# Performance work log

Measured on AMD Instinct MI355X. Metric: run time of the kernel, lower is better.

## Reference

```python
import jax, jax.numpy as jnp
import numpy as np

N, E = 50000, 1600000
IN, OUT, H = 128, 32, 2
NT, ET = 20, 4
ETE, EAE, ED = 16, 16, 16
SLOPE = 0.2  # conv_neg_slope


def setup_inputs() -> dict:
    key = jax.random.key(0)
    ks = jax.random.split(key, 11)
    d_att = 2 * OUT + ETE + EAE
    return dict(
        x=jax.random.normal(ks[0], (N, IN), jnp.float32),
        edge_index=jax.random.randint(ks[1], (2, E), 0, N),
        ntypes=jax.random.randint(ks[2], (N,), 0, NT),
        etypes=jax.random.randint(ks[3], (E,), 0, ET),
        eattr=jax.random.normal(ks[4], (E, ED), jnp.float32),
        het_W=jax.random.normal(ks[5], (NT, IN, OUT), jnp.float32) / np.sqrt(IN).astype(np.float32),
        het_b=jnp.zeros((NT, OUT), jnp.float32),
        etype_table=jax.random.normal(ks[6], (ET, ETE), jnp.float32),
        eattr_W=jax.random.normal(ks[7], (ED, EAE), jnp.float32) / np.sqrt(ED).astype(np.float32),
        att_W=jax.random.normal(ks[8], (d_att, H), jnp.float32) / np.sqrt(d_att).astype(np.float32),
        lin_W=jax.random.normal(ks[9], (OUT + EAE, OUT), jnp.float32) / np.sqrt(OUT + EAE).astype(np.float32),
    )


def _lrelu(v):
    return jax.nn.leaky_relu(v, SLOPE)


def _heat_conv(x, edge_index, ntypes, etypes, eattr,
               het_W, het_b, etype_table, eattr_W, att_W, lin_W):
    # HeteroLinear: node-type-conditioned linear transform (loop over 20 types,
    # avoids materializing a [N, IN, OUT] gathered-weight tensor)
    h = jnp.zeros((x.shape[0], het_W.shape[-1]), x.dtype)
    for t in range(het_W.shape[0]):
        h = h + jnp.where((ntypes == t)[:, None], x @ het_W[t] + het_b[t], 0.0)

    src, dst = edge_index[0], edge_index[1]
    ete = _lrelu(etype_table[etypes])        # [E, ETE] edge-type embedding
    ea = _lrelu(eattr @ eattr_W)             # [E, EAE] edge-attr embedding
    x_i = h[dst]                             # target node feats [E, OUT]
    x_j = h[src]                             # source node feats [E, OUT]

    feat = jnp.concatenate([x_i, x_j, ete, ea], axis=-1)
    alpha = _lrelu(feat @ att_W)             # [E, H] raw attention logits

    # softmax grouped by destination node, per head
    amax = jax.ops.segment_max(alpha, dst, num_segments=N)  # [N, H]
    alpha = jnp.exp(alpha - amax[dst])
    denom = jax.ops.segment_sum(alpha, dst, num_segments=N)  # [N, H]
    alpha = alpha / denom[dst]

    msg = jnp.concatenate([x_j, ea], axis=-1) @ lin_W        # [E, OUT]
    m = (msg[:, None, :] * alpha[:, :, None]).reshape(alpha.shape[0], H * OUT)
    out = jax.ops.segment_sum(m, dst, num_segments=N)        # [N, H*OUT]
    return out  # concat=True -> flattened heads


def reference(x, edge_index, ntypes, etypes, eattr,
              het_W, het_b, etype_table, eattr_W, att_W, lin_W):
    out = _heat_conv(x, edge_index, ntypes, etypes, eattr,
                     het_W, het_b, etype_table, eattr_W, att_W, lin_W)
    return jax.nn.relu(out)  # final activation in forward (eval mode: no dropout)
```

## Files before the change

kernel.cpp:

```cpp
#include <hip/hip_runtime.h>
#include <hip/hip_fp16.h>

#define NN 50000
#define EE 1600000
#define IN_F 128
#define OUT_F 32
#define SLOPE 0.2f
#define NB_SCAN 196

__global__ __launch_bounds__(256) void k_node(
    const float* __restrict__ x, const int* __restrict__ ntypes,
    const float* __restrict__ hetW, const float* __restrict__ hetb,
    const float* __restrict__ linW, const float* __restrict__ attW,
    float* __restrict__ hlin, float* __restrict__ auxS,
    float* __restrict__ auxD)
{
    __shared__ float sH[32 * 33];
    __shared__ float sLin[32 * 32];
    int tid = threadIdx.x;
    for (int i = tid; i < 1024; i += 256) sLin[i] = linW[i];

    int g = tid >> 3;
    int j = tid & 7;
    int n = blockIdx.x * 32 + g;
    int nc = n < NN ? n : NN - 1;
    int t = ntypes[nc];
    const float* W = hetW + (size_t)t * (IN_F * OUT_F);
    const float4* xr = (const float4*)(x + (size_t)nc * IN_F);

    float4 acc = ((const float4*)(hetb + t * OUT_F))[j];
    #pragma unroll 4
    for (int c = 0; c < 32; ++c) {
        float4 xv = xr[c];
        const float* Wr = W + (4 * c) * OUT_F + 4 * j;
        float4 w0 = *(const float4*)(Wr);
        float4 w1 = *(const float4*)(Wr + OUT_F);
        float4 w2 = *(const float4*)(Wr + 2 * OUT_F);
        float4 w3 = *(const float4*)(Wr + 3 * OUT_F);
        acc.x += xv.x * w0.x + xv.y * w1.x + xv.z * w2.x + xv.w * w3.x;
        acc.y += xv.x * w0.y + xv.y * w1.y + xv.z * w2.y + xv.w * w3.y;
        acc.z += xv.x * w0.z + xv.y * w1.z + xv.z * w2.z + xv.w * w3.z;
        acc.w += xv.x * w0.w + xv.y * w1.w + xv.z * w2.w + xv.w * w3.w;
    }
    sH[g * 33 + 4 * j + 0] = acc.x;
    sH[g * 33 + 4 * j + 1] = acc.y;
    sH[g * 33 + 4 * j + 2] = acc.z;
    sH[g * 33 + 4 * j + 3] = acc.w;
    __syncthreads();

    int o = tid & 31;
    #pragma unroll
    for (int pass = 0; pass < 4; ++pass) {
        int g2 = (tid >> 5) + 8 * pass;
        int n2 = blockIdx.x * 32 + g2;
        if (n2 >= NN) break;
        float accl = 0.0f;
        #pragma unroll
        for (int k = 0; k < 32; ++k)
            accl += sH[g2 * 33 + k] * sLin[k * 32 + o];
        hlin[(size_t)n2 * 32 + o] = accl;

        float hv = sH[g2 * 33 + o];
        float p0 = hv * attW[o * 2],        p1 = hv * attW[o * 2 + 1];
        float p2 = hv * attW[(32 + o) * 2], p3 = hv * attW[(32 + o) * 2 + 1];
        #pragma unroll
        for (int m = 16; m >= 1; m >>= 1) {
            p0 += __shfl_xor(p0, m, 32);
            p1 += __shfl_xor(p1, m, 32);
            p2 += __shfl_xor(p2, m, 32);
            p3 += __shfl_xor(p3, m, 32);
        }
        if (o == 0) {
            auxD[n2 * 2] = p0; auxD[n2 * 2 + 1] = p1;
            auxS[n2 * 2] = p2; auxS[n2 * 2 + 1] = p3;
        }
    }
}

__global__ __launch_bounds__(256) void k_count(
    const int* __restrict__ dst, int* __restrict__ count)
{
    int e = blockIdx.x * 256 + threadIdx.x;
    atomicAdd(&count[dst[e]], 1);
}

__global__ __launch_bounds__(256) void k_scanA(
    const int* __restrict__ count, int* __restrict__ offsets,
    int* __restrict__ bsum)
{
    __shared__ int s[256];
    int t = threadIdx.x;
    int i = blockIdx.x * 256 + t;
    int c = (i < NN) ? count[i] : 0;
    s[t] = c;
    __syncthreads();
    for (int off = 1; off < 256; off <<= 1) {
        int v = (t >= off) ? s[t - off] : 0;
        __syncthreads();
        s[t] += v;
        __syncthreads();
    }
    if (i < NN) offsets[i] = s[t] - c;
    if (t == 255) bsum[blockIdx.x] = s[255];
}

__global__ __launch_bounds__(256) void k_scanB(
    const int* __restrict__ bsum, int* __restrict__ bbase,
    const float* __restrict__ etab, const float* __restrict__ attW,
    float* __restrict__ etedot)
{
    __shared__ int s[256];
    int t = threadIdx.x;
    if (t < 8) {
        int et = t >> 1, hh = t & 1;
        float acc = 0.0f;
        for (int k = 0; k < 16; ++k) {
            float v = etab[et * 16 + k];
            v = v > 0.0f ? v : SLOPE * v;
            acc += v * attW[(64 + k) * 2 + hh];
        }
        etedot[t] = acc;
    }
    int c = (t < NB_SCAN) ? bsum[t] : 0;
    s[t] = c;
    __syncthreads();
    for (int off = 1; off < 256; off <<= 1) {
        int v = (t >= off) ? s[t - off] : 0;
        __syncthreads();
        s[t] += v;
        __syncthreads();
    }
    if (t < NB_SCAN) bbase[t] = s[t] - c;
}

__global__ __launch_bounds__(256) void k_scanC(
    int* __restrict__ offsets, const int* __restrict__ bbase,
    int* __restrict__ next)
{
    int t = threadIdx.x;
    int i = blockIdx.x * 256 + t;
    if (i < NN) {
        int v = offsets[i] + bbase[blockIdx.x];
        offsets[i] = v;
        next[i] = v;
    }
    if (i == 0) offsets[NN] = EE;
}

__global__ __launch_bounds__(256) void k_pre(
    const int* __restrict__ srcp, const int* __restrict__ dstp,
    const int* __restrict__ etypes, const float* __restrict__ eattr,
    const float* __restrict__ eaW, const float* __restrict__ attW,
    const float* __restrict__ etedot, const float* __restrict__ auxS,
    const float* __restrict__ auxD, int* __restrict__ next,
    int* __restrict__ srcS, int* __restrict__ dstS,
    float2* __restrict__ pS, __half* __restrict__ eaS)
{
    int e = blockIdx.x * 256 + threadIdx.x;
    int s = srcp[e], d = dstp[e], et = etypes[e];
    int slot = atomicAdd(&next[d], 1);

    float attr[16];
    {
        const float4* ap = (const float4*)(eattr + (size_t)e * 16);
        #pragma unroll
        for (int q = 0; q < 4; ++q) {
            float4 v = ap[q];
            attr[4*q+0] = v.x; attr[4*q+1] = v.y;
            attr[4*q+2] = v.z; attr[4*q+3] = v.w;
        }
    }
    float ea[16];
    #pragma unroll
    for (int j = 0; j < 16; ++j) {
        float acc = 0.0f;
        #pragma unroll
        for (int k = 0; k < 16; ++k) acc += attr[k] * eaW[k * 16 + j];
        ea[j] = acc > 0.0f ? acc : SLOPE * acc;
    }

    float2 aD = ((const float2*)auxD)[d];
    float2 aS = ((const float2*)auxS)[s];
    float2 eD = ((const float2*)etedot)[et];
    float al0 = aD.x + aS.x + eD.x;
    float al1 = aD.y + aS.y + eD.y;
    #pragma unroll
    for (int j = 0; j < 16; ++j) {
        al0 += ea[j] * attW[(80 + j) * 2];
        al1 += ea[j] * attW[(80 + j) * 2 + 1];
    }
    al0 = al0 > 0.0f ? al0 : SLOPE * al0;
    al1 = al1 > 0.0f ? al1 : SLOPE * al1;
    float p0 = __expf(al0), p1 = __expf(al1);

    srcS[slot] = s;
    dstS[slot] = d;
    pS[slot] = make_float2(p0, p1);
    __half2 eh[8];
    #pragma unroll
    for (int q = 0; q < 8; ++q) eh[q] = __floats2half2_rn(ea[2*q], ea[2*q+1]);
    float4* ep = (float4*)(eaS + (size_t)slot * 16);
    const float4* es = (const float4*)eh;
    ep[0] = es[0];
    ep[1] = es[1];
}

__global__ __launch_bounds__(256) void k_main2(
    const int* __restrict__ offsets, const int* __restrict__ srcS,
    const int* __restrict__ dstS, const float2* __restrict__ pS,
    const __half* __restrict__ eaS, const float* __restrict__ linW,
    const float* __restrict__ hlin,
    float* __restrict__ out, float* __restrict__ numbuf,
    float* __restrict__ denombuf)
{
    __shared__ float sMsg[256 * 33];
    __shared__ float sP[256 * 2];
    __shared__ int   sDst[256];
    __shared__ int   sWCnt[4];
    __shared__ int   sSegStart[256];
    __shared__ int   sSegNode[256];

    int tid = threadIdx.x;
    int s = blockIdx.x * 256 + tid;
    int src = srcS[s];
    int d   = dstS[s];
    float2 pp = pS[s];
    sDst[tid] = d;
    sP[tid * 2 + 0] = pp.x;
    sP[tid * 2 + 1] = pp.y;

    float ea[16];
    {
        const float4* ep = (const float4*)(eaS + (size_t)s * 16);
        float4 r0 = ep[0], r1 = ep[1];
        const __half2* eh0 = (const __half2*)&r0;
        const __half2* eh1 = (const __half2*)&r1;
        #pragma unroll
        for (int q = 0; q < 4; ++q) {
            float2 v = __half22float2(eh0[q]);
            ea[2*q] = v.x; ea[2*q+1] = v.y;
        }
        #pragma unroll
        for (int q = 0; q < 4; ++q) {
            float2 v = __half22float2(eh1[q]);
            ea[8+2*q] = v.x; ea[8+2*q+1] = v.y;
        }
    }

    float msg[32];
    {
        const float4* hp = (const float4*)(hlin + (size_t)src * 32);
        #pragma unroll
        for (int q = 0; q < 8; ++q) {
            float4 v = hp[q];
            msg[4*q+0] = v.x; msg[4*q+1] = v.y;
            msg[4*q+2] = v.z; msg[4*q+3] = v.w;
        }
    }
    #pragma unroll
    for (int j = 0; j < 16; ++j) {
        float e = ea[j];
        #pragma unroll
        for (int o = 0; o < 32; ++o) msg[o] += e * linW[(32 + j) * 32 + o];
    }
    #pragma unroll
    for (int o = 0; o < 32; ++o) sMsg[tid * 33 + o] = msg[o];
    __syncthreads();

    int ln = tid & 63, wv = tid >> 6;
    bool isStart = (tid == 0) || (sDst[tid - 1] != d);
    unsigned long long bm = __ballot(isStart);
    int wrank = __popcll(bm & ((1ull << ln) - 1ull));
    if (ln == 0) sWCnt[wv] = __popcll(bm);
    __syncthreads();
    int base = 0, nSeg = 0;
    #pragma unroll
    for (int w = 0; w < 4; ++w) {
        int c = sWCnt[w];
        if (w < wv) base += c;
        nSeg += c;
    }
    if (isStart) {
        int sid = base + wrank;
        sSegStart[sid] = tid;
        sSegNode[sid] = d;
    }
    __syncthreads();

    int o = ln & 31, hh = ln >> 5;
    int gs = blockIdx.x * 256;
    for (int g = wv; g < nSeg; g += 4) {
        int a = sSegStart[g];
        int b = (g + 1 < nSeg) ? sSegStart[g + 1] : 256;
        int n = sSegNode[g];
        float accm = 0.0f, accp = 0.0f;
        for (int tt = a; tt < b; ++tt) {
            float p = sP[tt * 2 + hh];
            accm += p * sMsg[tt * 33 + o];
            accp += p;
        }
        int o0 = offsets[n], o1 = offsets[n + 1];
        bool interior = (o0 == gs + a) && (o1 == gs + b);
        if (interior) {
            float v = accm / accp;
            out[(size_t)n * 64 + ln] = v > 0.0f ? v : 0.0f;
            if (o == 0) denombuf[n * 2 + hh] = -1.0f;
        } else {
            atomicAdd(&numbuf[(size_t)n * 64 + ln], accm);
            if (o == 0) atomicAdd(&denombuf[n * 2 + hh], accp);
        }
    }
}

__global__ __launch_bounds__(256) void k_final(
    float* __restrict__ out, const float* __restrict__ numbuf,
    const float* __restrict__ denombuf)
{
    int i = blockIdx.x * 256 + threadIdx.x;
    int n = i >> 6;
    int hh = (i >> 5) & 1;
    float dn = denombuf[n * 2 + hh];
    if (dn > 0.0f) {
        float v = numbuf[i] / dn;
        out[i] = v > 0.0f ? v : 0.0f;
    } else if (dn == 0.0f) {
        out[i] = 0.0f;
    }
}

extern "C" void kernel_launch(void* const* d_in, const int* in_sizes, int n_in,
                              void* d_out, int out_size, void* d_ws, size_t ws_size,
                              hipStream_t stream)
{
    const float* x      = (const float*)d_in[0];
    const int*   eidx   = (const int*)  d_in[1];
    const int*   ntypes = (const int*)  d_in[2];
    const int*   etypes = (const int*)  d_in[3];
    const float* eattr  = (const float*)d_in[4];
    const float* hetW   = (const float*)d_in[5];
    const float* hetb   = (const float*)d_in[6];
    const float* etab   = (const float*)d_in[7];
    const float* eaW    = (const float*)d_in[8];
    const float* attW   = (const float*)d_in[9];
    const float* linW   = (const float*)d_in[10];
    float* out = (float*)d_out;

    char* ws = (char*)d_ws;
    size_t off = 0;
    auto alloc = [&](size_t bytes) {
        char* p = ws + off;
        off = (off + bytes + 255) & ~(size_t)255;
        return p;
    };
    float*  hlin     = (float*) alloc((size_t)NN * 32 * sizeof(float));
    float*  auxS     = (float*) alloc((size_t)NN * 2 * sizeof(float));
    float*  auxD     = (float*) alloc((size_t)NN * 2 * sizeof(float));
    float*  etedot   = (float*) alloc(8 * sizeof(float));
    int*    count    = (int*)   alloc((size_t)NN * sizeof(int));
    int*    offsets  = (int*)   alloc(((size_t)NN + 1) * sizeof(int));
    int*    next     = (int*)   alloc((size_t)NN * sizeof(int));
    int*    bsum     = (int*)   alloc(256 * sizeof(int));
    int*    bbase    = (int*)   alloc(256 * sizeof(int));
    int*    srcS     = (int*)   alloc((size_t)EE * sizeof(int));
    int*    dstS     = (int*)   alloc((size_t)EE * sizeof(int));
    float2* pS       = (float2*)alloc((size_t)EE * sizeof(float2));
    __half* eaS      = (__half*)alloc((size_t)EE * 16 * sizeof(__half));
    float*  numbuf   = (float*) alloc((size_t)NN * 64 * sizeof(float));
    float*  denombuf = (float*) alloc((size_t)NN * 2 * sizeof(float));
    (void)ws_size;

    const int* srcp = eidx;
    const int* dstp = eidx + EE;

    hipMemsetAsync(count,    0, (size_t)NN * sizeof(int), stream);
    hipMemsetAsync(numbuf,   0, (size_t)NN * 64 * sizeof(float), stream);
    hipMemsetAsync(denombuf, 0, (size_t)NN * 2 * sizeof(float), stream);

    k_node<<<(NN + 31) / 32, 256, 0, stream>>>(x, ntypes, hetW, hetb, linW,
                                               attW, hlin, auxS, auxD);
    k_count<<<EE / 256, 256, 0, stream>>>(dstp, count);
    k_scanA<<<NB_SCAN, 256, 0, stream>>>(count, offsets, bsum);
    k_scanB<<<1, 256, 0, stream>>>(bsum, bbase, etab, attW, etedot);
    k_scanC<<<NB_SCAN, 256, 0, stream>>>(offsets, bbase, next);
    k_pre<<<EE / 256, 256, 0, stream>>>(srcp, dstp, etypes, eattr, eaW, attW,
                                        etedot, auxS, auxD, next,
                                        srcS, dstS, pS, eaS);
    k_main2<<<EE / 256, 256, 0, stream>>>(offsets, srcS, dstS, pS, eaS, linW,
                                          hlin, out, numbuf, denombuf);
    k_final<<<(NN * 64) / 256, 256, 0, stream>>>(out, numbuf, denombuf);
}
```

Baseline: 536.8 us.

## Replace per-node CSR sort with coarse bucket partition and shared-memory accumulation

Replaces the per-destination count/scan/scatter and the segmented reduction with a coarse bucketing scheme of 128 destination nodes per bucket. A single partition pass computes the full fp16 message and the attention weights, then writes a packed 80-byte payload per edge, using block-local ranks plus one global atomic per bucket. A second kernel accumulates each bucket in shared memory with LDS atomics and normalizes and ReLUs directly into the output. This removes the global numbuf/denombuf atomics, the final kernel and several launches, at the cost of a larger payload write and heavy LDS atomic contention in the accumulation pass.

Measured after the change: 1.125 ms. 110% more time.

```diff
diff --git a/kernel.cpp b/kernel.cpp
--- a/kernel.cpp
+++ b/kernel.cpp
@@ -4,9 +4,12 @@
 #define NN 50000
 #define EE 1600000
 #define IN_F 128
-#define OUT_F 32
 #define SLOPE 0.2f
-#define NB_SCAN 196
+#define BSH 7
+#define BNODES 128
+#define NBUCK 391
+#define P1_CHUNK 4096
+#define NB_P1 391
 
 __global__ __launch_bounds__(256) void k_node(
     const float* __restrict__ x, const int* __restrict__ ntypes,
@@ -25,18 +28,18 @@
     int n = blockIdx.x * 32 + g;
     int nc = n < NN ? n : NN - 1;
     int t = ntypes[nc];
-    const float* W = hetW + (size_t)t * (IN_F * OUT_F);
+    const float* W = hetW + (size_t)t * (IN_F * 32);
     const float4* xr = (const float4*)(x + (size_t)nc * IN_F);
 
-    float4 acc = ((const float4*)(hetb + t * OUT_F))[j];
+    float4 acc = ((const float4*)(hetb + t * 32))[j];
     #pragma unroll 4
     for (int c = 0; c < 32; ++c) {
         float4 xv = xr[c];
-        const float* Wr = W + (4 * c) * OUT_F + 4 * j;
+        const float* Wr = W + (4 * c) * 32 + 4 * j;
         float4 w0 = *(const float4*)(Wr);
-        float4 w1 = *(const float4*)(Wr + OUT_F);
-        float4 w2 = *(const float4*)(Wr + 2 * OUT_F);
-        float4 w3 = *(const float4*)(Wr + 3 * OUT_F);
+        float4 w1 = *(const float4*)(Wr + 32);
+        float4 w2 = *(const float4*)(Wr + 64);
+        float4 w3 = *(const float4*)(Wr + 96);
         acc.x += xv.x * w0.x + xv.y * w1.x + xv.z * w2.x + xv.w * w3.x;
         acc.y += xv.x * w0.y + xv.y * w1.y + xv.z * w2.y + xv.w * w3.y;
         acc.z += xv.x * w0.z + xv.y * w1.z + xv.z * w2.z + xv.w * w3.z;
@@ -77,39 +80,30 @@
     }
 }
 
-__global__ __launch_bounds__(256) void k_count(
-    const int* __restrict__ dst, int* __restrict__ count)
-{
-    int e = blockIdx.x * 256 + threadIdx.x;
-    atomicAdd(&count[dst[e]], 1);
-}
-
-__global__ __launch_bounds__(256) void k_scanA(
-    const int* __restrict__ count, int* __restrict__ offsets,
-    int* __restrict__ bsum)
-{
-    __shared__ int s[256];
-    int t = threadIdx.x;
-    int i = blockIdx.x * 256 + t;
-    int c = (i < NN) ? count[i] : 0;
-    s[t] = c;
-    __syncthreads();
-    for (int off = 1; off < 256; off <<= 1) {
-        int v = (t >= off) ? s[t - off] : 0;
-        __syncthreads();
-        s[t] += v;
-        __syncthreads();
-    }
-    if (i < NN) offsets[i] = s[t] - c;
-    if (t == 255) bsum[blockIdx.x] = s[255];
-}
-
-__global__ __launch_bounds__(256) void k_scanB(
-    const int* __restrict__ bsum, int* __restrict__ bbase,
-    const float* __restrict__ etab, const float* __restrict__ attW,
-    float* __restrict__ etedot)
-{
-    __shared__ int s[256];
+__global__ __launch_bounds__(512) void k_bhist(
+    const int* __restrict__ dst, int* __restrict__ bcount)
+{
+    __shared__ int lh[NBUCK];
+    int tid = threadIdx.x;
+    for (int i = tid; i < NBUCK; i += 512) lh[i] = 0;
+    __syncthreads();
+    int e0 = blockIdx.x * P1_CHUNK;
+    #pragma unroll
+    for (int k = 0; k < 8; ++k) {
+        int e = e0 + k * 512 + tid;
+        if (e < EE) atomicAdd(&lh[dst[e] >> BSH], 1);
+    }
+    __syncthreads();
+    for (int i = tid; i < NBUCK; i += 512)
+        if (lh[i]) atomicAdd(&bcount[i], lh[i]);
+}
+
+__global__ __launch_bounds__(512) void k_bscan(
+    const int* __restrict__ bcount, int* __restrict__ bbase,
+    int* __restrict__ cursor, const float* __restrict__ etab,
+    const float* __restrict__ attW, float* __restrict__ etedot)
+{
+    __shared__ int s[512];
     int t = threadIdx.x;
     if (t < 8) {
         int et = t >> 1, hh = t & 1;
@@ -121,210 +115,170 @@
         }
         etedot[t] = acc;
     }
-    int c = (t < NB_SCAN) ? bsum[t] : 0;
+    int c = (t < NBUCK) ? bcount[t] : 0;
     s[t] = c;
     __syncthreads();
-    for (int off = 1; off < 256; off <<= 1) {
+    for (int off = 1; off < 512; off <<= 1) {
         int v = (t >= off) ? s[t - off] : 0;
         __syncthreads();
         s[t] += v;
         __syncthreads();
     }
-    if (t < NB_SCAN) bbase[t] = s[t] - c;
-}
-
-__global__ __launch_bounds__(256) void k_scanC(
-    int* __restrict__ offsets, const int* __restrict__ bbase,
-    int* __restrict__ next)
-{
-    int t = threadIdx.x;
-    int i = blockIdx.x * 256 + t;
-    if (i < NN) {
-        int v = offsets[i] + bbase[blockIdx.x];
-        offsets[i] = v;
-        next[i] = v;
-    }
-    if (i == 0) offsets[NN] = EE;
-}
-
-__global__ __launch_bounds__(256) void k_pre(
+    if (t < NBUCK) {
+        int b = s[t] - c;
+        bbase[t] = b;
+        cursor[t] = b;
+    }
+    if (t == 0) bbase[NBUCK] = EE;
+}
+
+__global__ __launch_bounds__(512) void k_p1(
     const int* __restrict__ srcp, const int* __restrict__ dstp,
     const int* __restrict__ etypes, const float* __restrict__ eattr,
     const float* __restrict__ eaW, const float* __restrict__ attW,
-    const float* __restrict__ etedot, const float* __restrict__ auxS,
-    const float* __restrict__ auxD, int* __restrict__ next,
-    int* __restrict__ srcS, int* __restrict__ dstS,
-    float2* __restrict__ pS, __half* __restrict__ eaS)
-{
-    int e = blockIdx.x * 256 + threadIdx.x;
-    int s = srcp[e], d = dstp[e], et = etypes[e];
-    int slot = atomicAdd(&next[d], 1);
-
-    float attr[16];
-    {
-        const float4* ap = (const float4*)(eattr + (size_t)e * 16);
-        #pragma unroll
-        for (int q = 0; q < 4; ++q) {
-            float4 v = ap[q];
-            attr[4*q+0] = v.x; attr[4*q+1] = v.y;
-            attr[4*q+2] = v.z; attr[4*q+3] = v.w;
-        }
-    }
-    float ea[16];
+    const float* __restrict__ linW, const float* __restrict__ etedot,
+    const float* __restrict__ auxS, const float* __restrict__ auxD,
+    const float* __restrict__ hlin, int* __restrict__ cursor,
+    float4* __restrict__ payload)
+{
+    __shared__ int lh[NBUCK];
+    __shared__ int lbase[NBUCK];
+    int tid = threadIdx.x;
+    for (int i = tid; i < NBUCK; i += 512) lh[i] = 0;
+    __syncthreads();
+
+    int e0 = blockIdx.x * P1_CHUNK;
+    int myrank[8], myb[8];
     #pragma unroll
-    for (int j = 0; j < 16; ++j) {
-        float acc = 0.0f;
-        #pragma unroll
-        for (int k = 0; k < 16; ++k) acc += attr[k] * eaW[k * 16 + j];
-        ea[j] = acc > 0.0f ? acc : SLOPE * acc;
-    }
-
-    float2 aD = ((const float2*)auxD)[d];
-    float2 aS = ((const float2*)auxS)[s];
-    float2 eD = ((const float2*)etedot)[et];
-    float al0 = aD.x + aS.x + eD.x;
-    float al1 = aD.y + aS.y + eD.y;
-    #pragma unroll
-    for (int j = 0; j < 16; ++j) {
-        al0 += ea[j] * attW[(80 + j) * 2];
-        al1 += ea[j] * attW[(80 + j) * 2 + 1];
-    }
-    al0 = al0 > 0.0f ? al0 : SLOPE * al0;
-    al1 = al1 > 0.0f ? al1 : SLOPE * al1;
-    float p0 = __expf(al0), p1 = __expf(al1);
-
-    srcS[slot] = s;
-    dstS[slot] = d;
-    pS[slot] = make_float2(p0, p1);
-    __half2 eh[8];
-    #pragma unroll
-    for (int q = 0; q < 8; ++q) eh[q] = __floats2half2_rn(ea[2*q], ea[2*q+1]);
-    float4* ep = (float4*)(eaS + (size_t)slot * 16);
-    const float4* es = (const float4*)eh;
-    ep[0] = es[0];
-    ep[1] = es[1];
-}
-
-__global__ __launch_bounds__(256) void k_main2(
-    const int* __restrict__ offsets, const int* __restrict__ srcS,
-    const int* __restrict__ dstS, const float2* __restrict__ pS,
-    const __half* __restrict__ eaS, const float* __restrict__ linW,
-    const float* __restrict__ hlin,
-    float* __restrict__ out, float* __restrict__ numbuf,
-    float* __restrict__ denombuf)
-{
-    __shared__ float sMsg[256 * 33];
-    __shared__ float sP[256 * 2];
-    __shared__ int   sDst[256];
-    __shared__ int   sWCnt[4];
-    __shared__ int   sSegStart[256];
-    __shared__ int   sSegNode[256];
-
+    for (int k = 0; k < 8; ++k) {
+        int e = e0 + k * 512 + tid;
+        if (e >= EE) break;
+        int b = dstp[e] >> BSH;
+        myb[k] = b;
+        myrank[k] = atomicAdd(&lh[b], 1);
+    }
+    __syncthreads();
+    for (int i = tid; i < NBUCK; i += 512) {
+        int c = lh[i];
+        lbase[i] = c ? atomicAdd(&cursor[i], c) : 0;
+    }
+    __syncthreads();
+
+    for (int k = 0; k < 8; ++k) {
+        int e = e0 + k * 512 + tid;
+        if (e >= EE) break;
+        int s = srcp[e], d = dstp[e], et = etypes[e];
+
+        float attr[16];
+        {
+            const float4* ap = (const float4*)(eattr + (size_t)e * 16);
+            #pragma unroll
+            for (int q = 0; q < 4; ++q) {
+                float4 v = ap[q];
+                attr[4*q+0] = v.x; attr[4*q+1] = v.y;
+                attr[4*q+2] = v.z; attr[4*q+3] = v.w;
+            }
+        }
+        float ea[16];
+        #pragma unroll
+        for (int j = 0; j < 16; ++j) {
+            float acc = 0.0f;
+            #pragma unroll
+            for (int kk = 0; kk < 16; ++kk) acc += attr[kk] * eaW[kk * 16 + j];
+            ea[j] = acc > 0.0f ? acc : SLOPE * acc;
+        }
+
+        float2 aD = ((const float2*)auxD)[d];
+        float2 aS = ((const float2*)auxS)[s];
+        float2 eD = ((const float2*)etedot)[et];
+        float al0 = aD.x + aS.x + eD.x;
+        float al1 = aD.y + aS.y + eD.y;
+        #pragma unroll
+        for (int j = 0; j < 16; ++j) {
+            al0 += ea[j] * attW[(80 + j) * 2];
+            al1 += ea[j] * attW[(80 + j) * 2 + 1];
+        }
+        al0 = al0 > 0.0f ? al0 : SLOPE * al0;
+        al1 = al1 > 0.0f ? al1 : SLOPE * al1;
+        float p0 = __expf(al0), p1 = __expf(al1);
+
+        float msg[32];
+        {
+            const float4* hp = (const float4*)(hlin + (size_t)s * 32);
+            #pragma unroll
+            for (int q = 0; q < 8; ++q) {
+                float4 v = hp[q];
+                msg[4*q+0] = v.x; msg[4*q+1] = v.y;
+                msg[4*q+2] = v.z; msg[4*q+3] = v.w;
+            }
+        }
+        #pragma unroll
+        for (int j = 0; j < 16; ++j) {
+            float ej = ea[j];
+            #pragma unroll
+            for (int o = 0; o < 32; ++o) msg[o] += ej * linW[(32 + j) * 32 + o];
+        }
+
+        int slot = lbase[myb[k]] + myrank[k];
+        float4* P = payload + (size_t)slot * 5;
+        P[0] = make_float4(__int_as_float(d & (BNODES - 1)), p0, p1, 0.0f);
+        __half2 mh[16];
+        #pragma unroll
+        for (int q = 0; q < 16; ++q)
+            mh[q] = __floats2half2_rn(msg[2*q], msg[2*q+1]);
+        const float4* ms = (const float4*)mh;
+        P[1] = ms[0]; P[2] = ms[1]; P[3] = ms[2]; P[4] = ms[3];
+    }
+}
+
+__global__ __launch_bounds__(512) void k_p2(
+    const float4* __restrict__ payload, const int* __restrict__ bbase,
+    float* __restrict__ out)
+{
+    __shared__ float sNum[BNODES * 65];
+    __shared__ float sDen[BNODES * 2];
     int tid = threadIdx.x;
-    int s = blockIdx.x * 256 + tid;
-    int src = srcS[s];
-    int d   = dstS[s];
-    float2 pp = pS[s];
-    sDst[tid] = d;
-    sP[tid * 2 + 0] = pp.x;
-    sP[tid * 2 + 1] = pp.y;
-
-    float ea[16];
-    {
-        const float4* ep = (const float4*)(eaS + (size_t)s * 16);
-        float4 r0 = ep[0], r1 = ep[1];
-        const __half2* eh0 = (const __half2*)&r0;
-        const __half2* eh1 = (const __half2*)&r1;
-        #pragma unroll
-        for (int q = 0; q < 4; ++q) {
-            float2 v = __half22float2(eh0[q]);
-            ea[2*q] = v.x; ea[2*q+1] = v.y;
-        }
-        #pragma unroll
-        for (int q = 0; q < 4; ++q) {
-            float2 v = __half22float2(eh1[q]);
-            ea[8+2*q] = v.x; ea[8+2*q+1] = v.y;
-        }
-    }
-
-    float msg[32];
-    {
-        const float4* hp = (const float4*)(hlin + (size_t)src * 32);
-        #pragma unroll
-        for (int q = 0; q < 8; ++q) {
-            float4 v = hp[q];
-            msg[4*q+0] = v.x; msg[4*q+1] = v.y;
-            msg[4*q+2] = v.z; msg[4*q+3] = v.w;
-        }
-    }
-    #pragma unroll
-    for (int j = 0; j < 16; ++j) {
-        float e = ea[j];
-        #pragma unroll
-        for (int o = 0; o < 32; ++o) msg[o] += e * linW[(32 + j) * 32 + o];
-    }
-    #pragma unroll
-    for (int o = 0; o < 32; ++o) sMsg[tid * 33 + o] = msg[o];
-    __syncthreads();
-
-    int ln = tid & 63, wv = tid >> 6;
-    bool isStart = (tid == 0) || (sDst[tid - 1] != d);
-    unsigned long long bm = __ballot(isStart);
-    int wrank = __popcll(bm & ((1ull << ln) - 1ull));
-    if (ln == 0) sWCnt[wv] = __popcll(bm);
-    __syncthreads();
-    int base = 0, nSeg = 0;
-    #pragma unroll
-    for (int w = 0; w < 4; ++w) {
-        int c = sWCnt[w];
-        if (w < wv) base += c;
-        nSeg += c;
-    }
-    if (isStart) {
-        int sid = base + wrank;
-        sSegStart[sid] = tid;
-        sSegNode[sid] = d;
-    }
-    __syncthreads();
-
-    int o = ln & 31, hh = ln >> 5;
-    int gs = blockIdx.x * 256;
-    for (int g = wv; g < nSeg; g += 4) {
-        int a = sSegStart[g];
-        int b = (g + 1 < nSeg) ? sSegStart[g + 1] : 256;
-        int n = sSegNode[g];
-        float accm = 0.0f, accp = 0.0f;
-        for (int tt = a; tt < b; ++tt) {
-            float p = sP[tt * 2 + hh];
-            accm += p * sMsg[tt * 33 + o];
-            accp += p;
-        }
-        int o0 = offsets[n], o1 = offsets[n + 1];
-        bool interior = (o0 == gs + a) && (o1 == gs + b);
-        if (interior) {
-            float v = accm / accp;
-            out[(size_t)n * 64 + ln] = v > 0.0f ? v : 0.0f;
-            if (o == 0) denombuf[n * 2 + hh] = -1.0f;
-        } else {
-            atomicAdd(&numbuf[(size_t)n * 64 + ln], accm);
-            if (o == 0) atomicAdd(&denombuf[n * 2 + hh], accp);
-        }
-    }
-}
-
-__global__ __launch_bounds__(256) void k_final(
-    float* __restrict__ out, const float* __restrict__ numbuf,
-    const float* __restrict__ denombuf)
-{
-    int i = blockIdx.x * 256 + threadIdx.x;
-    int n = i >> 6;
-    int hh = (i >> 5) & 1;
-    float dn = denombuf[n * 2 + hh];
-    if (dn > 0.0f) {
-        float v = numbuf[i] / dn;
-        out[i] = v > 0.0f ? v : 0.0f;
-    } else if (dn == 0.0f) {
-        out[i] = 0.0f;
+    for (int i = tid; i < BNODES * 65; i += 512) sNum[i] = 0.0f;
+    for (int i = tid; i < BNODES * 2; i += 512) sDen[i] = 0.0f;
+    __syncthreads();
+
+    int b = blockIdx.x;
+    int s0 = bbase[b], s1 = bbase[b + 1];
+
+    for (int e = s0 + tid; e < s1; e += 512) {
+        const float4* P = payload + (size_t)e * 5;
+        float4 h0 = P[0];
+        float4 r0 = P[1], r1 = P[2], r2 = P[3], r3 = P[4];
+        int dl = __float_as_int(h0.x);
+        float p0 = h0.y, p1 = h0.z;
+        float m[32];
+        {
+            float4 regs[4] = {r0, r1, r2, r3};
+            const __half2* hp = (const __half2*)regs;
+            #pragma unroll
+            for (int q = 0; q < 16; ++q) {
+                float2 v = __half22float2(hp[q]);
+                m[2*q] = v.x; m[2*q+1] = v.y;
+            }
+        }
+        float* row = &sNum[dl * 65];
+        #pragma unroll
+        for (int c = 0; c < 32; ++c) atomicAdd(&row[c], p0 * m[c]);
+        #pragma unroll
+        for (int c = 0; c < 32; ++c) atomicAdd(&row[32 + c], p1 * m[c]);
+        atomicAdd(&sDen[dl * 2 + 0], p0);
+        atomicAdd(&sDen[dl * 2 + 1], p1);
+    }
+    __syncthreads();
+
+    int n0 = b * BNODES;
+    for (int i = tid; i < BNODES * 64; i += 512) {
+        int node = i >> 6, ch = i & 63;
+        int n = n0 + node;
+        if (n >= NN) continue;
+        float den = sDen[node * 2 + (ch >> 5)];
+        float v = den > 0.0f ? sNum[node * 65 + ch] / den : 0.0f;
+        out[(size_t)n * 64 + ch] = v > 0.0f ? v : 0.0f;
     }
 }
 
@@ -352,40 +306,27 @@
         off = (off + bytes + 255) & ~(size_t)255;
         return p;
     };
-    float*  hlin     = (float*) alloc((size_t)NN * 32 * sizeof(float));
-    float*  auxS     = (float*) alloc((size_t)NN * 2 * sizeof(float));
-    float*  auxD     = (float*) alloc((size_t)NN * 2 * sizeof(float));
-    float*  etedot   = (float*) alloc(8 * sizeof(float));
-    int*    count    = (int*)   alloc((size_t)NN * sizeof(int));
-    int*    offsets  = (int*)   alloc(((size_t)NN + 1) * sizeof(int));
-    int*    next     = (int*)   alloc((size_t)NN * sizeof(int));
-    int*    bsum     = (int*)   alloc(256 * sizeof(int));
-    int*    bbase    = (int*)   alloc(256 * sizeof(int));
-    int*    srcS     = (int*)   alloc((size_t)EE * sizeof(int));
-    int*    dstS     = (int*)   alloc((size_t)EE * sizeof(int));
-    float2* pS       = (float2*)alloc((size_t)EE * sizeof(float2));
-    __half* eaS      = (__half*)alloc((size_t)EE * 16 * sizeof(__half));
-    float*  numbuf   = (float*) alloc((size_t)NN * 64 * sizeof(float));
-    float*  denombuf = (float*) alloc((size_t)NN * 2 * sizeof(float));
+    float*  hlin    = (float*) alloc((size_t)NN * 32 * sizeof(float));
+    float*  auxS    = (float*) alloc((size_t)NN * 2 * sizeof(float));
+    float*  auxD    = (float*) alloc((size_t)NN * 2 * sizeof(float));
+    float*  etedot  = (float*) alloc(8 * sizeof(float));
+    int*    bcount  = (int*)   alloc(NBUCK * sizeof(int));
+    int*    bbase   = (int*)   alloc((NBUCK + 1) * sizeof(int));
+    int*    cursor  = (int*)   alloc(NBUCK * sizeof(int));
+    float4* payload = (float4*)alloc((size_t)EE * 5 * sizeof(float4));
     (void)ws_size;
 
     const int* srcp = eidx;
     const int* dstp = eidx + EE;
 
-    hipMemsetAsync(count,    0, (size_t)NN * sizeof(int), stream);
-    hipMemsetAsync(numbuf,   0, (size_t)NN * 64 * sizeof(float), stream);
-    hipMemsetAsync(denombuf, 0, (size_t)NN * 2 * sizeof(float), stream);
+    hipMemsetAsync(bcount, 0, NBUCK * sizeof(int), stream);
 
     k_node<<<(NN + 31) / 32, 256, 0, stream>>>(x, ntypes, hetW, hetb, linW,
                                                attW, hlin, auxS, auxD);
-    k_count<<<EE / 256, 256, 0, stream>>>(dstp, count);
-    k_scanA<<<NB_SCAN, 256, 0, stream>>>(count, offsets, bsum);
-    k_scanB<<<1, 256, 0, stream>>>(bsum, bbase, etab, attW, etedot);
-    k_scanC<<<NB_SCAN, 256, 0, stream>>>(offsets, bbase, next);
-    k_pre<<<EE / 256, 256, 0, stream>>>(srcp, dstp, etypes, eattr, eaW, attW,
-                                        etedot, auxS, auxD, next,
-                                        srcS, dstS, pS, eaS);
-    k_main2<<<EE / 256, 256, 0, stream>>>(offsets, srcS, dstS, pS, eaS, linW,
-                                          hlin, out, numbuf, denombuf);
-    k_final<<<(NN * 64) / 256, 256, 0, stream>>>(out, numbuf, denombuf);
-}
+    k_bhist<<<NB_P1, 512, 0, stream>>>(dstp, bcount);
+    k_bscan<<<1, 512, 0, stream>>>(bcount, bbase, cursor, etab, attW, etedot);
+    k_p1<<<NB_P1, 512, 0, stream>>>(srcp, dstp, etypes, eattr, eaW, attW,
+                                    linW, etedot, auxS, auxD, hlin, cursor,
+                                    payload);
+    k_p2<<<NBUCK, 512, 0, stream>>>(payload, bbase, out);
+}
```

## Compute full messages in scatter pass and reduce per node with CSR gather

Applied to the files above, without the earlier changes.

The edge pre-pass now computes the full 32-wide message (gathered hlin row plus the projected edge-attribute term) and writes it in fp32, together with the unnormalised attention weights, into destination-sorted slots. A new per-node gather kernel walks each node's CSR range, accumulates the weighted messages and weights, normalises, and applies ReLU. This removes the segmented shared-memory reduction, the atomics into numbuf/denombuf, their memsets, and the final normalisation kernel. In exchange it writes and reads a 1.6M×32 fp32 message buffer (about 200 MB each way), where the old path stored fp16 edge attributes, and the scattered slot writes become much wider.

Result: slower. 579.0 us (+7.9%).

```diff
diff --git a/kernel.cpp b/kernel.cpp
--- a/kernel.cpp
+++ b/kernel.cpp
@@ -1,10 +1,8 @@
 #include <hip/hip_runtime.h>
-#include <hip/hip_fp16.h>
 
 #define NN 50000
 #define EE 1600000
 #define IN_F 128
-#define OUT_F 32
 #define SLOPE 0.2f
 #define NB_SCAN 196
 
@@ -25,18 +23,18 @@
     int n = blockIdx.x * 32 + g;
     int nc = n < NN ? n : NN - 1;
     int t = ntypes[nc];
-    const float* W = hetW + (size_t)t * (IN_F * OUT_F);
+    const float* W = hetW + (size_t)t * (IN_F * 32);
     const float4* xr = (const float4*)(x + (size_t)nc * IN_F);
 
-    float4 acc = ((const float4*)(hetb + t * OUT_F))[j];
+    float4 acc = ((const float4*)(hetb + t * 32))[j];
     #pragma unroll 4
     for (int c = 0; c < 32; ++c) {
         float4 xv = xr[c];
-        const float* Wr = W + (4 * c) * OUT_F + 4 * j;
+        const float* Wr = W + (4 * c) * 32 + 4 * j;
         float4 w0 = *(const float4*)(Wr);
-        float4 w1 = *(const float4*)(Wr + OUT_F);
-        float4 w2 = *(const float4*)(Wr + 2 * OUT_F);
-        float4 w3 = *(const float4*)(Wr + 3 * OUT_F);
+        float4 w1 = *(const float4*)(Wr + 32);
+        float4 w2 = *(const float4*)(Wr + 64);
+        float4 w3 = *(const float4*)(Wr + 96);
         acc.x += xv.x * w0.x + xv.y * w1.x + xv.z * w2.x + xv.w * w3.x;
         acc.y += xv.x * w0.y + xv.y * w1.y + xv.z * w2.y + xv.w * w3.y;
         acc.z += xv.x * w0.z + xv.y * w1.z + xv.z * w2.z + xv.w * w3.z;
@@ -147,14 +145,14 @@
     if (i == 0) offsets[NN] = EE;
 }
 
-__global__ __launch_bounds__(256) void k_pre(
+__global__ __launch_bounds__(256) void k_pre2(
     const int* __restrict__ srcp, const int* __restrict__ dstp,
     const int* __restrict__ etypes, const float* __restrict__ eattr,
     const float* __restrict__ eaW, const float* __restrict__ attW,
-    const float* __restrict__ etedot, const float* __restrict__ auxS,
-    const float* __restrict__ auxD, int* __restrict__ next,
-    int* __restrict__ srcS, int* __restrict__ dstS,
-    float2* __restrict__ pS, __half* __restrict__ eaS)
+    const float* __restrict__ linW, const float* __restrict__ etedot,
+    const float* __restrict__ auxS, const float* __restrict__ auxD,
+    const float* __restrict__ hlin, int* __restrict__ next,
+    float* __restrict__ msgbuf, float2* __restrict__ pbuf)
 {
     int e = blockIdx.x * 256 + threadIdx.x;
     int s = srcp[e], d = dstp[e], et = etypes[e];
@@ -193,63 +191,9 @@
     al1 = al1 > 0.0f ? al1 : SLOPE * al1;
     float p0 = __expf(al0), p1 = __expf(al1);
 
-    srcS[slot] = s;
-    dstS[slot] = d;
-    pS[slot] = make_float2(p0, p1);
-    __half2 eh[8];
-    #pragma unroll
-    for (int q = 0; q < 8; ++q) eh[q] = __floats2half2_rn(ea[2*q], ea[2*q+1]);
-    float4* ep = (float4*)(eaS + (size_t)slot * 16);
-    const float4* es = (const float4*)eh;
-    ep[0] = es[0];
-    ep[1] = es[1];
-}
-
-__global__ __launch_bounds__(256) void k_main2(
-    const int* __restrict__ offsets, const int* __restrict__ srcS,
-    const int* __restrict__ dstS, const float2* __restrict__ pS,
-    const __half* __restrict__ eaS, const float* __restrict__ linW,
-    const float* __restrict__ hlin,
-    float* __restrict__ out, float* __restrict__ numbuf,
-    float* __restrict__ denombuf)
-{
-    __shared__ float sMsg[256 * 33];
-    __shared__ float sP[256 * 2];
-    __shared__ int   sDst[256];
-    __shared__ int   sWCnt[4];
-    __shared__ int   sSegStart[256];
-    __shared__ int   sSegNode[256];
-
-    int tid = threadIdx.x;
-    int s = blockIdx.x * 256 + tid;
-    int src = srcS[s];
-    int d   = dstS[s];
-    float2 pp = pS[s];
-    sDst[tid] = d;
-    sP[tid * 2 + 0] = pp.x;
-    sP[tid * 2 + 1] = pp.y;
-
-    float ea[16];
-    {
-        const float4* ep = (const float4*)(eaS + (size_t)s * 16);
-        float4 r0 = ep[0], r1 = ep[1];
-        const __half2* eh0 = (const __half2*)&r0;
-        const __half2* eh1 = (const __half2*)&r1;
-        #pragma unroll
-        for (int q = 0; q < 4; ++q) {
-            float2 v = __half22float2(eh0[q]);
-            ea[2*q] = v.x; ea[2*q+1] = v.y;
-        }
-        #pragma unroll
-        for (int q = 0; q < 4; ++q) {
-            float2 v = __half22float2(eh1[q]);
-            ea[8+2*q] = v.x; ea[8+2*q+1] = v.y;
-        }
-    }
-
     float msg[32];
     {
-        const float4* hp = (const float4*)(hlin + (size_t)src * 32);
+        const float4* hp = (const float4*)(hlin + (size_t)s * 32);
         #pragma unroll
         for (int q = 0; q < 8; ++q) {
             float4 v = hp[q];
@@ -259,73 +203,51 @@
     }
     #pragma unroll
     for (int j = 0; j < 16; ++j) {
-        float e = ea[j];
-        #pragma unroll
-        for (int o = 0; o < 32; ++o) msg[o] += e * linW[(32 + j) * 32 + o];
-    }
-    #pragma unroll
-    for (int o = 0; o < 32; ++o) sMsg[tid * 33 + o] = msg[o];
-    __syncthreads();
-
-    int ln = tid & 63, wv = tid >> 6;
-    bool isStart = (tid == 0) || (sDst[tid - 1] != d);
-    unsigned long long bm = __ballot(isStart);
-    int wrank = __popcll(bm & ((1ull << ln) - 1ull));
-    if (ln == 0) sWCnt[wv] = __popcll(bm);
-    __syncthreads();
-    int base = 0, nSeg = 0;
-    #pragma unroll
-    for (int w = 0; w < 4; ++w) {
-        int c = sWCnt[w];
-        if (w < wv) base += c;
-        nSeg += c;
-    }
-    if (isStart) {
-        int sid = base + wrank;
-        sSegStart[sid] = tid;
-        sSegNode[sid] = d;
-    }
-    __syncthreads();
-
-    int o = ln & 31, hh = ln >> 5;
-    int gs = blockIdx.x * 256;
-    for (int g = wv; g < nSeg; g += 4) {
-        int a = sSegStart[g];
-        int b = (g + 1 < nSeg) ? sSegStart[g + 1] : 256;
-        int n = sSegNode[g];
-        float accm = 0.0f, accp = 0.0f;
-        for (int tt = a; tt < b; ++tt) {
-            float p = sP[tt * 2 + hh];
-            accm += p * sMsg[tt * 33 + o];
-            accp += p;
-        }
-        int o0 = offsets[n], o1 = offsets[n + 1];
-        bool interior = (o0 == gs + a) && (o1 == gs + b);
-        if (interior) {
-            float v = accm / accp;
-            out[(size_t)n * 64 + ln] = v > 0.0f ? v : 0.0f;
-            if (o == 0) denombuf[n * 2 + hh] = -1.0f;
-        } else {
-            atomicAdd(&numbuf[(size_t)n * 64 + ln], accm);
-            if (o == 0) atomicAdd(&denombuf[n * 2 + hh], accp);
-        }
-    }
-}
-
-__global__ __launch_bounds__(256) void k_final(
-    float* __restrict__ out, const float* __restrict__ numbuf,
-    const float* __restrict__ denombuf)
-{
-    int i = blockIdx.x * 256 + threadIdx.x;
-    int n = i >> 6;
-    int hh = (i >> 5) & 1;
-    float dn = denombuf[n * 2 + hh];
-    if (dn > 0.0f) {
-        float v = numbuf[i] / dn;
-        out[i] = v > 0.0f ? v : 0.0f;
-    } else if (dn == 0.0f) {
-        out[i] = 0.0f;
-    }
+        float ej = ea[j];
+        #pragma unroll
+        for (int o = 0; o < 32; ++o) msg[o] += ej * linW[(32 + j) * 32 + o];
+    }
+
+    pbuf[slot] = make_float2(p0, p1);
+    float4* mp = (float4*)(msgbuf + (size_t)slot * 32);
+    const float4* ms = (const float4*)msg;
+    #pragma unroll
+    for (int q = 0; q < 8; ++q) mp[q] = ms[q];
+}
+
+__global__ __launch_bounds__(256) void k_gather2(
+    const int* __restrict__ offsets, const float* __restrict__ msgbuf,
+    const float2* __restrict__ pbuf, float* __restrict__ out)
+{
+    int tid = blockIdx.x * 256 + threadIdx.x;
+    int n = tid >> 6;
+    int lane = tid & 63;
+    if (n >= NN) return;
+    int o = lane & 31, hh = lane >> 5;
+    int s0 = offsets[n], s1 = offsets[n + 1];
+
+    float accm = 0.0f, accp = 0.0f;
+    int slot = s0;
+    for (; slot + 1 < s1; slot += 2) {
+        float m0 = msgbuf[(size_t)slot * 32 + o];
+        float2 pv0 = pbuf[slot];
+        float m1 = msgbuf[(size_t)(slot + 1) * 32 + o];
+        float2 pv1 = pbuf[slot + 1];
+        float p0 = hh ? pv0.y : pv0.x;
+        float p1 = hh ? pv1.y : pv1.x;
+        accm += m0 * p0;
+        accm += m1 * p1;
+        accp += p0 + p1;
+    }
+    if (slot < s1) {
+        float m0 = msgbuf[(size_t)slot * 32 + o];
+        float2 pv0 = pbuf[slot];
+        float p0 = hh ? pv0.y : pv0.x;
+        accm += m0 * p0;
+        accp += p0;
+    }
+    float v = accp > 0.0f ? accm / accp : 0.0f;
+    out[(size_t)n * 64 + lane] = v > 0.0f ? v : 0.0f;
 }
 
 extern "C" void kernel_launch(void* const* d_in, const int* in_sizes, int n_in,
@@ -352,29 +274,23 @@
         off = (off + bytes + 255) & ~(size_t)255;
         return p;
     };
-    float*  hlin     = (float*) alloc((size_t)NN * 32 * sizeof(float));
-    float*  auxS     = (float*) alloc((size_t)NN * 2 * sizeof(float));
-    float*  auxD     = (float*) alloc((size_t)NN * 2 * sizeof(float));
-    float*  etedot   = (float*) alloc(8 * sizeof(float));
-    int*    count    = (int*)   alloc((size_t)NN * sizeof(int));
-    int*    offsets  = (int*)   alloc(((size_t)NN + 1) * sizeof(int));
-    int*    next     = (int*)   alloc((size_t)NN * sizeof(int));
-    int*    bsum     = (int*)   alloc(256 * sizeof(int));
-    int*    bbase    = (int*)   alloc(256 * sizeof(int));
-    int*    srcS     = (int*)   alloc((size_t)EE * sizeof(int));
-    int*    dstS     = (int*)   alloc((size_t)EE * sizeof(int));
-    float2* pS       = (float2*)alloc((size_t)EE * sizeof(float2));
-    __half* eaS      = (__half*)alloc((size_t)EE * 16 * sizeof(__half));
-    float*  numbuf   = (float*) alloc((size_t)NN * 64 * sizeof(float));
-    float*  denombuf = (float*) alloc((size_t)NN * 2 * sizeof(float));
+    float*  hlin    = (float*) alloc((size_t)NN * 32 * sizeof(float));
+    float*  auxS    = (float*) alloc((size_t)NN * 2 * sizeof(float));
+    float*  auxD    = (float*) alloc((size_t)NN * 2 * sizeof(float));
+    float*  etedot  = (float*) alloc(8 * sizeof(float));
+    int*    count   = (int*)   alloc((size_t)NN * sizeof(int));
+    int*    offsets = (int*)   alloc(((size_t)NN + 1) * sizeof(int));
+    int*    next    = (int*)   alloc((size_t)NN * sizeof(int));
+    int*    bsum    = (int*)   alloc(256 * sizeof(int));
+    int*    bbase   = (int*)   alloc(256 * sizeof(int));
+    float2* pbuf    = (float2*)alloc((size_t)EE * sizeof(float2));
+    float*  msgbuf  = (float*) alloc((size_t)EE * 32 * sizeof(float));
     (void)ws_size;
 
     const int* srcp = eidx;
     const int* dstp = eidx + EE;
 
-    hipMemsetAsync(count,    0, (size_t)NN * sizeof(int), stream);
-    hipMemsetAsync(numbuf,   0, (size_t)NN * 64 * sizeof(float), stream);
-    hipMemsetAsync(denombuf, 0, (size_t)NN * 2 * sizeof(float), stream);
+    hipMemsetAsync(count, 0, (size_t)NN * sizeof(int), stream);
 
     k_node<<<(NN + 31) / 32, 256, 0, stream>>>(x, ntypes, hetW, hetb, linW,
                                                attW, hlin, auxS, auxD);
@@ -382,10 +298,8 @@
     k_scanA<<<NB_SCAN, 256, 0, stream>>>(count, offsets, bsum);
     k_scanB<<<1, 256, 0, stream>>>(bsum, bbase, etab, attW, etedot);
     k_scanC<<<NB_SCAN, 256, 0, stream>>>(offsets, bbase, next);
-    k_pre<<<EE / 256, 256, 0, stream>>>(srcp, dstp, etypes, eattr, eaW, attW,
-                                        etedot, auxS, auxD, next,
-                                        srcS, dstS, pS, eaS);
-    k_main2<<<EE / 256, 256, 0, stream>>>(offsets, srcS, dstS, pS, eaS, linW,
-                                          hlin, out, numbuf, denombuf);
-    k_final<<<(NN * 64) / 256, 256, 0, stream>>>(out, numbuf, denombuf);
-}
+    k_pre2<<<EE / 256, 256, 0, stream>>>(srcp, dstp, etypes, eattr, eaW, attW,
+                                         linW, etedot, auxS, auxD, hlin, next,
+                                         msgbuf, pbuf);
+    k_gather2<<<(NN * 64 + 255) / 256, 256, 0, stream>>>(offsets, msgbuf, pbuf, out);
+}
```
